# Performance work log

Measured on AMD Instinct MI355X. Metric: run time of the kernel, lower is better.

Reference implementation:

```python
import jax, jax.numpy as jnp
import numpy as np
import math

B, N, D = 64, 128, 128          # graphs, nodes per graph, d_model
D_STATE = 2                     # Mamba default d_state
D_CONV = 4                      # Mamba default conv kernel
DT_RANK = math.ceil(D / 16)     # 8
CUTOFF = 10.0
N_GAUSS = 50                    # GaussianSmearing(0, 10, 50)
EPS_RMS = 1e-5


def setup_inputs() -> dict:
    key = jax.random.key(0)
    ks = jax.random.split(key, 12)
    s = 0.05
    inp = {}
    inp['x'] = jax.random.normal(ks[0], (B * N, D), jnp.float32)
    inp['pos'] = jax.random.normal(ks[1], (B * N, 3), jnp.float32) * 5.0
    inp['map_idx'] = jax.random.randint(ks[2], (B * N,), 0, 16)
    inp['batch'] = jnp.repeat(jnp.arange(B), N)
    # RMSNorm
    inp['norm_w'] = jnp.ones((D,), jnp.float32)
    # simple message-passing gnn (stand-in for injected gnn module)
    inp['gnn_w1'] = jax.random.normal(ks[3], (D, D), jnp.float32) * s
    inp['gnn_b1'] = jnp.zeros((D,), jnp.float32)
    inp['gnn_w2'] = jax.random.normal(ks[4], (D, D), jnp.float32) * s
    inp['gnn_b2'] = jnp.zeros((D,), jnp.float32)
    # Linear(50, 1) on Gaussian-smeared edge distances
    inp['lin_w'] = jax.random.normal(ks[5], (N_GAUSS, 1), jnp.float32) * s
    inp['lin_b'] = jnp.zeros((1,), jnp.float32)
    # MambaBlock params (stored [in, out])
    inp['in_proj_w'] = jax.random.normal(ks[6], (D, 2 * D), jnp.float32) * s
    inp['conv_w'] = jax.random.normal(ks[7], (D, D_CONV), jnp.float32) * s
    inp['conv_b'] = jnp.zeros((D,), jnp.float32)
    inp['x_proj_w'] = jax.random.normal(ks[8], (D, DT_RANK + 2 * D_STATE), jnp.float32) * s
    inp['dt_proj_w'] = jax.random.normal(ks[9], (DT_RANK, D), jnp.float32) * s
    inp['dt_proj_b'] = jnp.zeros((D,), jnp.float32)
    inp['A_log'] = jnp.log(jnp.tile(jnp.arange(1, D_STATE + 1, dtype=jnp.float32), (D, 1)))
    inp['D_param'] = jnp.ones((D,), jnp.float32)
    inp['out_proj_w'] = jax.random.normal(ks[10], (D, D), jnp.float32) * s
    return inp


def _rmsnorm(x, w):
    return x * jax.lax.rsqrt(jnp.mean(x * x, axis=-1, keepdims=True) + EPS_RMS) * w


def _mamba(x_t, adj, in_proj_w, conv_w, conv_b, x_proj_w, dt_proj_w, dt_proj_b,
           A_log, D_param, out_proj_w):
    # x_t: [N, D] node sequence for one graph; adj: [N, N] dense edge-value matrix
    L = x_t.shape[0]
    A = -jnp.exp(A_log)                                   # [D, S]
    xr = x_t @ in_proj_w                                  # [L, 2D]
    xm, res = xr[:, :D], xr[:, D:]
    # causal depthwise conv1d (padding d_conv-1, truncated to L)
    xp = jnp.pad(xm, ((D_CONV - 1, 0), (0, 0)))
    xc = conv_b + sum(xp[j:j + L] * conv_w[:, j] for j in range(D_CONV))
    xc = jax.nn.silu(xc)                                  # [L, D]
    dbl = xc @ x_proj_w                                   # [L, dt_rank + 2S]
    delta = dbl[:, :DT_RANK]
    Bm = dbl[:, DT_RANK:DT_RANK + D_STATE]                # [L, S]
    Cm = dbl[:, DT_RANK + D_STATE:]                       # [L, S]
    delta = jax.nn.softplus(delta @ dt_proj_w + dt_proj_b)  # [L, D]
    # temp_adj_padded: ones [D, D] with adjacency slice in top-left
    m = min(L, D)
    adj_pad = jnp.ones((D, D), dtype=adj.dtype).at[:m, :m].set(adj[:m, :m])
    delta_p = delta @ adj_pad                             # [L, D]
    dA = jnp.exp(delta_p[:, :, None] * A[None])           # [L, D, S]
    dBu = delta_p[:, :, None] * Bm[:, None, :] * xc[:, :, None]

    def step(h, t):
        dA_t, dBu_t, C_t = t
        h = dA_t * h + dBu_t                              # [D, S]
        return h, h @ C_t                                 # [D]

    _, ys = jax.lax.scan(step, jnp.zeros((D, D_STATE), x_t.dtype), (dA, dBu, Cm))
    y = ys + xc * D_param
    y = y * jax.nn.silu(res)
    out = y @ out_proj_w
    return jnp.where(jnp.isfinite(out), out, 0.0)


def reference(x, pos, map_idx, batch, norm_w, gnn_w1, gnn_b1, gnn_w2, gnn_b2,
              lin_w, lin_b, in_proj_w, conv_w, conv_b, x_proj_w, dt_proj_w,
              dt_proj_b, A_log, D_param, out_proj_w):
    x1 = _rmsnorm(x, norm_w)                              # [B*N, D]
    xg = x1.reshape(B, N, D)
    pg = pos.reshape(B, N, 3)
    # per-graph radius graph (dense): dist + edge mask
    diff = pg[:, :, None, :] - pg[:, None, :, :]          # [B, N, N, 3]
    d2 = jnp.sum(diff * diff, axis=-1)
    eye = jnp.eye(N, dtype=bool)[None]
    dist = jnp.sqrt(jnp.where(eye, 1.0, d2))              # safe sqrt on diag
    edge_mask = (~eye) & (dist < CUTOFF)                  # [B, N, N]
    em = edge_mask.astype(x1.dtype)
    # simple message-passing gnn: mean-aggregate relu(Wx) over radius neighbors
    h = jax.nn.relu(xg @ gnn_w1 + gnn_b1)
    deg = jnp.clip(jnp.sum(em, axis=-1, keepdims=True), 1.0, None)
    agg = jnp.einsum('bij,bjd->bid', em, h) / deg
    x2 = agg @ gnn_w2 + gnn_b2                            # [B, N, D]
    # GaussianSmearing(0, 10, 50) + Linear(50, 1) -> dense edge-value matrix
    offsets = jnp.linspace(0.0, 10.0, N_GAUSS)
    coeff = -0.5 / (offsets[1] - offsets[0]) ** 2
    smear = jnp.exp(coeff * (dist[..., None] - offsets) ** 2)  # [B, N, N, 50]
    d_dense = smear @ lin_w[:, 0] + lin_b[0]
    adj = jnp.where(edge_mask, d_dense, 0.0)              # sparse-to-dense
    # Mamba mixer over each graph's node sequence
    mix = jax.vmap(lambda xt, a: _mamba(xt, a, in_proj_w, conv_w, conv_b,
                                        x_proj_w, dt_proj_w, dt_proj_b,
                                        A_log, D_param, out_proj_w))
    x3 = mix(x2, adj).reshape(B * N, D)
    output = x3 + x1
    return (output, pos, map_idx)
```

## Files before the change

### kernel.cpp

```cpp
#include <hip/hip_runtime.h>
#include <math.h>

#define B_ 64
#define N_ 128
#define D_ 128
#define BN_ 8192
#define NG_ 50
#define CUTOFF_ 10.0f

typedef __attribute__((ext_vector_type(8))) short short8v;
typedef __attribute__((ext_vector_type(4))) float f32x4;
#define MFMA16 __builtin_amdgcn_mfma_f32_16x16x32_bf16

__device__ __forceinline__ float bf2f(unsigned short h) {
    return __builtin_bit_cast(float, ((unsigned int)h) << 16);
}
__device__ __forceinline__ unsigned short f2bf(float f) {
    unsigned int u = __builtin_bit_cast(unsigned int, f);
    return (unsigned short)((u + 0x7FFFu + ((u >> 16) & 1u)) >> 16);
}
__device__ __forceinline__ void splitbf(float x, unsigned short& h, unsigned short& l) {
    h = f2bf(x);
    l = f2bf(x - bf2f(h));
}
__device__ __forceinline__ void gl_lds(const void* g, void* l) {
    __builtin_amdgcn_global_load_lds(
        (const __attribute__((address_space(1))) void*)g,
        (__attribute__((address_space(3))) void*)l, 16, 0, 0);
}

__global__ __launch_bounds__(256) void setup_k(
        const float* __restrict__ x, const float* __restrict__ norm_w,
        const float* __restrict__ pos, const int* __restrict__ mi,
        const float* __restrict__ lin_w, const float* __restrict__ lin_b,
        const float* __restrict__ w1, const float* __restrict__ w2,
        const float* __restrict__ b2, const float* __restrict__ in_proj,
        const float* __restrict__ xpw, const float* __restrict__ dtw,
        const float* __restrict__ out_proj,
        unsigned short* __restrict__ w1Th, unsigned short* __restrict__ w1Tl,
        unsigned short* __restrict__ WdTh, unsigned short* __restrict__ WdTl,
        unsigned short* __restrict__ opTh, unsigned short* __restrict__ opTl,
        unsigned short* __restrict__ WfTh, unsigned short* __restrict__ WfTl,
        float* __restrict__ bfv,
        float* __restrict__ x1f, unsigned short* __restrict__ x1h,
        unsigned short* __restrict__ x1l,
        unsigned short* __restrict__ adjh, unsigned short* __restrict__ adjl,
        unsigned short* __restrict__ emh, float* __restrict__ rdeg,
        float* __restrict__ out) {
    int blk = blockIdx.x, t = threadIdx.x;
    if (blk < 513) {
        if (blk < 128) {
            if (t < 128) {
                unsigned short h, l;
                splitbf(w1[blk * 128 + t], h, l);
                w1Th[t * 128 + blk] = h; w1Tl[t * 128 + blk] = l;
            }
        } else if (blk < 256) {
            int m = blk - 128;
            if (t < 128) {
                float s = 0.0f;
                #pragma unroll
                for (int r = 0; r < 8; r++) s = fmaf(xpw[m * 12 + r], dtw[r * 128 + t], s);
                unsigned short h, l; splitbf(s, h, l);
                WdTh[t * 128 + m] = h; WdTl[t * 128 + m] = l;
            }
        } else if (blk < 384) {
            int k = blk - 256;
            if (t < 128) {
                unsigned short h, l;
                splitbf(out_proj[k * 128 + t], h, l);
                opTh[t * 128 + k] = h; opTl[t * 128 + k] = l;
            }
        } else if (blk < 512) {
            int k = blk - 384;
            float s = 0.0f;
            #pragma unroll 8
            for (int j = 0; j < 128; j++) s = fmaf(w2[k * 128 + j], in_proj[j * 256 + t], s);
            unsigned short h, l; splitbf(s, h, l);
            WfTh[t * 128 + k] = h; WfTl[t * 128 + k] = l;
        } else {
            float s = 0.0f;
            #pragma unroll 8
            for (int j = 0; j < 128; j++) s = fmaf(b2[j], in_proj[j * 256 + t], s);
            bfv[t] = s;
        }
    } else if (blk < 642) {
        int idx = (blk - 513) * 256 + t;
        if (idx < BN_ * 3) out[(size_t)BN_ * D_ + idx] = pos[idx];
        if (idx < BN_) out[(size_t)BN_ * D_ + BN_ * 3 + idx] = (float)mi[idx];
    } else if (blk < 2690) {
        int rblk = blk - 642;
        int wv = t >> 6, ln = t & 63;
        int row = rblk * 4 + wv;
        const float2* xr = reinterpret_cast<const float2*>(x) + (size_t)row * 64;
        float2 v = xr[ln];
        float s = fmaf(v.x, v.x, v.y * v.y);
        #pragma unroll
        for (int o = 32; o > 0; o >>= 1) s += __shfl_down(s, o, 64);
        float tot = __shfl(s, 0, 64);
        float r = rsqrtf(tot * (1.0f / D_) + 1e-5f);
        float2 wv2 = reinterpret_cast<const float2*>(norm_w)[ln];
        float o0 = v.x * r * wv2.x, o1 = v.y * r * wv2.y;
        reinterpret_cast<float2*>(x1f)[(size_t)row * 64 + ln] = make_float2(o0, o1);
        unsigned short h0, l0, h1, l1;
        splitbf(o0, h0, l0); splitbf(o1, h1, l1);
        reinterpret_cast<ushort2*>(x1h)[(size_t)row * 64 + ln] = make_ushort2(h0, h1);
        reinterpret_cast<ushort2*>(x1l)[(size_t)row * 64 + ln] = make_ushort2(l0, l1);
    } else {
        __shared__ float px[N_], py[N_], pz[N_];
        __shared__ float lw[NG_];
        __shared__ int degs[8];
        int ablk = blk - 2690;
        int bx = ablk & 15, b = ablk >> 4;
        if (t < N_) {
            const float* p = pos + (size_t)(b * N_ + t) * 3;
            px[t] = p[0]; py[t] = p[1]; pz[t] = p[2];
        } else if (t - N_ < NG_) {
            lw[t - N_] = lin_w[t - N_];
        }
        if (t >= 248) degs[t - 248] = 0;
        __syncthreads();
        float linb = lin_b[0];
        int j = t & 127;
        int il = t >> 7;
        const float DEL = 10.0f / 49.0f;
        const float COEFF = -0.5f / (DEL * DEL);
        #pragma unroll
        for (int p = 0; p < 4; p++) {
            int i = bx * 8 + p * 2 + il;
            float dx = px[i] - px[j], dy = py[i] - py[j], dz = pz[i] - pz[j];
            float d2 = dx * dx + dy * dy + dz * dz;
            float dist = (i == j) ? 1.0f : sqrtf(d2);
            bool edge = (i != j) && (dist < CUTOFF_);
            float val = 0.0f;
            if (edge) {
                int g0 = (int)ceilf((dist - 1.75f) / DEL); if (g0 < 0) g0 = 0;
                int g1 = (int)floorf((dist + 1.75f) / DEL); if (g1 > NG_ - 1) g1 = NG_ - 1;
                float s = linb;
                for (int g = g0; g <= g1; g++) {
                    float tt = dist - (float)g * DEL;
                    s += lw[g] * expf(COEFF * tt * tt);
                }
                val = s;
            }
            size_t idx = ((size_t)b * N_ + i) * N_ + j;
            unsigned short h, l; splitbf(val, h, l);
            adjh[idx] = h; adjl[idx] = l;
            emh[idx] = edge ? 0x3F80 : 0;
            unsigned long long msk = __ballot(edge);
            if ((t & 63) == 0) atomicAdd(&degs[p * 2 + il], __popcll(msk));
        }
        __syncthreads();
        if (t < 8) {
            int dg = degs[t];
            rdeg[(size_t)b * N_ + bx * 8 + t] = 1.0f / (float)(dg > 0 ? dg : 1);
        }
    }
}

#define AHOFF 0
#define ALOFF 8192
#define BHOFF 16384
#define BLOFF 32768
template <int EPI, bool ALO>
__global__ __launch_bounds__(256, 3) void mgemm_k(
        const unsigned short* __restrict__ Ah, const unsigned short* __restrict__ Al,
        const unsigned short* __restrict__ BTh, const unsigned short* __restrict__ BTl,
        const float* __restrict__ bias, const float* __restrict__ AUX,
        float* __restrict__ Cf, unsigned short* __restrict__ Ch,
        unsigned short* __restrict__ Cl, float* __restrict__ Cf2,
        int cstride, int wbs) {
    extern __shared__ char sm[];
    int tid = threadIdx.x;
    int row_base = blockIdx.x * 32;
    int col_base = blockIdx.y * 64;

    const unsigned short* pBh = BTh;
    const unsigned short* pBl = BTl;
    if (wbs) {
        size_t bo = (size_t)(row_base >> 7) * (size_t)wbs;
        pBh += bo; pBl += bo;
    }

    #pragma unroll
    for (int i = 0; i < 2; i++) {
        int s = tid + i * 256;
        int row = s >> 4, inner = s & 15;
        int gb = (inner * 16) ^ ((row & 7) << 4);
        size_t gsrc = (size_t)(row_base + row) * 256 + gb;
        gl_lds((const char*)Ah + gsrc, sm + AHOFF + s * 16);
        if (ALO) gl_lds((const char*)Al + gsrc, sm + ALOFF + s * 16);
    }
    #pragma unroll
    for (int i = 0; i < 4; i++) {
        int s = tid + i * 256;
        int n = s >> 4, inner = s & 15;
        int gb = (inner * 16) ^ ((n & 7) << 4);
        size_t gsrc = (size_t)(col_base + n) * 256 + gb;
        gl_lds((const char*)pBh + gsrc, sm + BHOFF + s * 16);
        gl_lds((const char*)pBl + gsrc, sm + BLOFF + s * 16);
    }
    __syncthreads();

    int w = tid >> 6, l = tid & 63;
    int rlow = l & 15, kb_lane = (l >> 4) * 16;
    int nB = w * 16 + rlow;
    int nswz = (nB & 7) << 4;
    f32x4 acc[2] = {{0.f, 0.f, 0.f, 0.f}, {0.f, 0.f, 0.f, 0.f}};
    #pragma unroll
    for (int kb = 0; kb < 4; kb++) {
        int kbyte = kb * 64 + kb_lane;
        short8v bh = *(const short8v*)(sm + BHOFF + nB * 256 + (kbyte ^ nswz));
        short8v bl = *(const short8v*)(sm + BLOFF + nB * 256 + (kbyte ^ nswz));
        #pragma unroll
        for (int rf = 0; rf < 2; rf++) {
            int ra = rf * 16 + rlow;
            int aswz = (ra & 7) << 4;
            short8v ah = *(const short8v*)(sm + AHOFF + ra * 256 + (kbyte ^ aswz));
            acc[rf] = MFMA16(ah, bh, acc[rf], 0, 0, 0);
            acc[rf] = MFMA16(ah, bl, acc[rf], 0, 0, 0);
            if (ALO) {
                short8v al_ = *(const short8v*)(sm + ALOFF + ra * 256 + (kbyte ^ aswz));
                acc[rf] = MFMA16(al_, bh, acc[rf], 0, 0, 0);
            }
        }
    }

    int colg = col_base + w * 16 + rlow;
    #pragma unroll
    for (int rf = 0; rf < 2; rf++) {
        int row0 = row_base + rf * 16 + (l >> 4) * 4;
        if (EPI == 1) {
            float b_ = bias[colg];
            unsigned short hh[4], ll[4];
            #pragma unroll
            for (int q = 0; q < 4; q++) {
                float t = fmaxf(acc[rf][q] + b_, 0.0f);
                splitbf(t, hh[q], ll[q]);
            }
            size_t bb = (size_t)(row0 >> 7) * 16384 + (size_t)colg * 128 + (row0 & 127);
            *reinterpret_cast<ushort4*>(Ch + bb) = make_ushort4(hh[0], hh[1], hh[2], hh[3]);
            *reinterpret_cast<ushort4*>(Cl + bb) = make_ushort4(ll[0], ll[1], ll[2], ll[3]);
        } else if (EPI == 7) {
            size_t bb = ((size_t)(row0 >> 7) * 128 + colg) * 128 + (row0 & 127);
            *reinterpret_cast<float4*>(Cf + bb) =
                make_float4(acc[rf][0], acc[rf][1], acc[rf][2], acc[rf][3]);
        } else if (EPI == 6 && colg >= 128) {
            float b_ = bias[colg];
            float v[4];
            #pragma unroll
            for (int q = 0; q < 4; q++) {
                float rs = acc[rf][q] + b_;
                v[q] = rs / (1.0f + expf(-rs));
            }
            size_t bb = ((size_t)(row0 >> 7) * 128 + (colg - 128)) * 128 + (row0 & 127);
            *reinterpret_cast<float4*>(Cf2 + bb) = make_float4(v[0], v[1], v[2], v[3]);
        } else {
            #pragma unroll
            for (int q = 0; q < 4; q++) {
                int row = row0 + q;
                float t = acc[rf][q];
                if (EPI == 2) {
                    t *= AUX[row];
                    unsigned short h, lo; splitbf(t, h, lo);
                    Ch[(size_t)row * 128 + colg] = h;
                    Cl[(size_t)row * 128 + colg] = lo;
                }
                if (EPI == 4) {
                    t += bias[colg];
                    t = fmaxf(t, 0.0f) + log1pf(expf(-fabsf(t)));
                    unsigned short h, lo; splitbf(t, h, lo);
                    Ch[(size_t)row * 128 + colg] = h;
                    Cl[(size_t)row * 128 + colg] = lo;
                }
                if (EPI == 5) {
                    t = isfinite(t) ? t : 0.0f;
                    t += AUX[(size_t)row * 128 + colg];
                    Cf[(size_t)row * cstride + colg] = t;
                }
                if (EPI == 6) {
                    t += bias[colg];
                    Cf[(size_t)row * 128 + colg] = t;
                }
            }
        }
    }
}

__global__ __launch_bounds__(256) void convsm_k(const float* __restrict__ xm,
                                                const float* __restrict__ conv_w,
                                                const float* __restrict__ conv_b,
                                                const float* __restrict__ xpw,
                                                unsigned short* __restrict__ xch,
                                                unsigned short* __restrict__ xcl,
                                                float* __restrict__ xcT,
                                                float* __restrict__ bcT) {
    int tid = threadIdx.x;
    int slot = tid >> 7;
    int d = tid & 127;
    int ln = tid & 63;
    int wv = (tid >> 6) & 1;
    __shared__ float red[2][2][4];
    __shared__ float xcs[4][128];
    float cw[4];
    #pragma unroll
    for (int jj = 0; jj < 4; jj++) cw[jj] = conv_w[d * 4 + jj];
    float cb = conv_b[d];
    float4 wv4 = *reinterpret_cast<const float4*>(xpw + d * 12 + 8);

    #pragma unroll
    for (int it = 0; it < 2; it++) {
        int row = blockIdx.x * 4 + it * 2 + slot;
        int bt = row & 127;
        float accv = cb;
        #pragma unroll
        for (int jj = 0; jj < 4; jj++) {
            int tt = bt + jj - 3;
            if (tt >= 0) accv = fmaf(xm[((size_t)(row + jj - 3)) * 128 + d], cw[jj], accv);
        }
        float xcv = accv / (1.0f + expf(-accv));
        xcs[it * 2 + slot][d] = xcv;
        unsigned short h, lo; splitbf(xcv, h, lo);
        xch[(size_t)row * D_ + d] = h;
        xcl[(size_t)row * D_ + d] = lo;
        float p0 = xcv * wv4.x, p1 = xcv * wv4.y, p2 = xcv * wv4.z, p3 = xcv * wv4.w;
        #pragma unroll
        for (int o = 32; o > 0; o >>= 1) {
            p0 += __shfl_down(p0, o, 64);
            p1 += __shfl_down(p1, o, 64);
            p2 += __shfl_down(p2, o, 64);
            p3 += __shfl_down(p3, o, 64);
        }
        if (ln == 0) {
            red[slot][wv][0] = p0; red[slot][wv][1] = p1;
            red[slot][wv][2] = p2; red[slot][wv][3] = p3;
        }
        __syncthreads();
        if (d < 4) {
            int b = row >> 7;
            bcT[(size_t)b * 512 + d * 128 + (row & 127)] = red[slot][0][d] + red[slot][1][d];
        }
        __syncthreads();
    }
    if (tid < 128) {
        int b = blockIdx.x >> 5;
        int t0 = (blockIdx.x * 4) & 127;
        float4 v = make_float4(xcs[0][tid], xcs[1][tid], xcs[2][tid], xcs[3][tid]);
        *reinterpret_cast<float4*>(xcT + ((size_t)b * 128 + tid) * 128 + t0) = v;
    }
}

__global__ __launch_bounds__(256) void scan_k(const float* __restrict__ dpT,
                                              const float* __restrict__ xcT,
                                              const float* __restrict__ bcT,
                                              const float* __restrict__ resT,
                                              const float* __restrict__ A_log,
                                              const float* __restrict__ Dpar,
                                              unsigned short* __restrict__ yh,
                                              unsigned short* __restrict__ yl) {
    int g = blockIdx.x * 256 + threadIdx.x;
    int b = g >> 7, d = g & 127;
    float a1 = -expf(A_log[d * 2]);
    float a2 = -expf(A_log[d * 2 + 1]);
    float Dp = Dpar[d];
    const float4* dp4 = reinterpret_cast<const float4*>(dpT + ((size_t)b * 128 + d) * 128);
    const float4* xc4 = reinterpret_cast<const float4*>(xcT + ((size_t)b * 128 + d) * 128);
    const float4* rr4 = reinterpret_cast<const float4*>(resT + ((size_t)b * 128 + d) * 128);
    const float4* b04 = reinterpret_cast<const float4*>(bcT + (size_t)b * 512);
    const float4* b14 = b04 + 32;
    const float4* c04 = b04 + 64;
    const float4* c14 = b04 + 96;
    float h1 = 0.0f, h2 = 0.0f;
    size_t ybase = (size_t)b * 16384 + d;
    #pragma unroll 4
    for (int tc = 0; tc < 32; tc++) {
        float4 dp = dp4[tc], xc = xc4[tc], rr = rr4[tc];
        float4 bm0 = b04[tc], bm1 = b14[tc], cm0 = c04[tc], cm1 = c14[tc];
        #pragma unroll
        for (int q = 0; q < 4; q++) {
            float dpv = (q == 0) ? dp.x : (q == 1) ? dp.y : (q == 2) ? dp.z : dp.w;
            float xcv = (q == 0) ? xc.x : (q == 1) ? xc.y : (q == 2) ? xc.z : xc.w;
            float rv  = (q == 0) ? rr.x : (q == 1) ? rr.y : (q == 2) ? rr.z : rr.w;
            float bmv0 = (q == 0) ? bm0.x : (q == 1) ? bm0.y : (q == 2) ? bm0.z : bm0.w;
            float bmv1 = (q == 0) ? bm1.x : (q == 1) ? bm1.y : (q == 2) ? bm1.z : bm1.w;
            float cmv0 = (q == 0) ? cm0.x : (q == 1) ? cm0.y : (q == 2) ? cm0.z : cm0.w;
            float cmv1 = (q == 0) ? cm1.x : (q == 1) ? cm1.y : (q == 2) ? cm1.z : cm1.w;
            float e1 = expf(dpv * a1), e2 = expf(dpv * a2);
            float bu = dpv * xcv;
            h1 = fmaf(e1, h1, bu * bmv0);
            h2 = fmaf(e2, h2, bu * bmv1);
            float y = fmaf(h1, cmv0, h2 * cmv1);
            float yv = fmaf(xcv, Dp, y) * rv;
            unsigned short hh, ll; splitbf(yv, hh, ll);
            int t = tc * 4 + q;
            yh[ybase + (size_t)t * 128] = hh;
            yl[ybase + (size_t)t * 128] = ll;
        }
    }
}

extern "C" void kernel_launch(void* const* d_in, const int* in_sizes, int n_in,
                              void* d_out, int out_size, void* d_ws, size_t ws_size,
                              hipStream_t stream) {
    const float* x        = (const float*)d_in[0];
    const float* pos      = (const float*)d_in[1];
    const int*   mi       = (const int*)d_in[2];
    const float* norm_w   = (const float*)d_in[4];
    const float* w1       = (const float*)d_in[5];
    const float* b1       = (const float*)d_in[6];
    const float* w2       = (const float*)d_in[7];
    const float* b2       = (const float*)d_in[8];
    const float* lin_w    = (const float*)d_in[9];
    const float* lin_b    = (const float*)d_in[10];
    const float* in_proj  = (const float*)d_in[11];
    const float* conv_w   = (const float*)d_in[12];
    const float* conv_b   = (const float*)d_in[13];
    const float* xpw      = (const float*)d_in[14];
    const float* dtw      = (const float*)d_in[15];
    const float* dtb      = (const float*)d_in[16];
    const float* A_log    = (const float*)d_in[17];
    const float* Dpar     = (const float*)d_in[18];
    const float* out_proj = (const float*)d_in[19];

    float* out = (float*)d_out;
    char* base = (char*)d_ws;
    const size_t MB = 1u << 20;
    const size_t PL = 1048576;

    float* x1f  = (float*)(base);
    float* xm   = (float*)(base + 4 * MB);
    float* resT = (float*)(base + 8 * MB);
    float* dpT  = (float*)(base + 12 * MB);
    float* xcT  = (float*)(base + 16 * MB);
    float* bcT  = (float*)(base + 20 * MB);
    float* rdeg = (float*)(base + 20 * MB + 131072);

    unsigned short* P = (unsigned short*)(base + 21 * MB);
    unsigned short* x1h  = P +  0 * PL;
    unsigned short* x1l  = P +  1 * PL;
    unsigned short* hTh  = P +  2 * PL;
    unsigned short* hTl  = P +  3 * PL;
    unsigned short* aggh = P +  4 * PL;
    unsigned short* aggl = P +  5 * PL;
    unsigned short* xch  = P +  6 * PL;
    unsigned short* xcl  = P +  7 * PL;
    unsigned short* dlh  = P +  8 * PL;
    unsigned short* dll  = P +  9 * PL;
    unsigned short* yh   = P + 10 * PL;
    unsigned short* yl   = P + 11 * PL;
    unsigned short* adjh = P + 12 * PL;
    unsigned short* adjl = P + 13 * PL;
    unsigned short* emh  = P + 14 * PL;

    unsigned short* W = (unsigned short*)(base + 52 * MB);
    unsigned short* w1Th = W;
    unsigned short* w1Tl = W + 16384;
    unsigned short* WdTh = W + 2 * 16384;
    unsigned short* WdTl = W + 3 * 16384;
    unsigned short* opTh = W + 4 * 16384;
    unsigned short* opTl = W + 5 * 16384;
    unsigned short* WfTh = W + 6 * 16384;
    unsigned short* WfTl = WfTh + 32768;
    float* bfv = (float*)(WfTl + 32768);

    const size_t gsm = 49152;

    setup_k<<<3714, 256, 0, stream>>>(x, norm_w, pos, mi, lin_w, lin_b,
                                      w1, w2, b2, in_proj, xpw, dtw, out_proj,
                                      w1Th, w1Tl, WdTh, WdTl, opTh, opTl, WfTh, WfTl,
                                      bfv, x1f, x1h, x1l, adjh, adjl, emh, rdeg, out);
    mgemm_k<1, true><<<dim3(256, 2), 256, gsm, stream>>>(
        x1h, x1l, w1Th, w1Tl, b1, nullptr, nullptr, hTh, hTl, nullptr, 128, 0);
    mgemm_k<2, false><<<dim3(256, 2), 256, gsm, stream>>>(
        emh, emh, hTh, hTl, nullptr, rdeg, nullptr, aggh, aggl, nullptr, 128, 16384);
    mgemm_k<6, true><<<dim3(256, 4), 256, gsm, stream>>>(
        aggh, aggl, WfTh, WfTl, bfv, nullptr, xm, nullptr, nullptr, resT, 128, 0);
    convsm_k<<<2048, 256, 0, stream>>>(xm, conv_w, conv_b, xpw, xch, xcl, xcT, bcT);
    mgemm_k<4, true><<<dim3(256, 2), 256, gsm, stream>>>(
        xch, xcl, WdTh, WdTl, dtb, nullptr, nullptr, dlh, dll, nullptr, 128, 0);
    mgemm_k<7, true><<<dim3(256, 2), 256, gsm, stream>>>(
        dlh, dll, adjh, adjl, nullptr, nullptr, dpT, nullptr, nullptr, nullptr, 128, 16384);
    scan_k<<<32, 256, 0, stream>>>(dpT, xcT, bcT, resT, A_log, Dpar, yh, yl);
    mgemm_k<5, true><<<dim3(256, 2), 256, gsm, stream>>>(
        yh, yl, opTh, opTl, nullptr, x1f, out, nullptr, nullptr, nullptr, 128, 0);
}
```

Baseline: 95.70 us.

## Fuse in_proj, conv+SiLU, dt projection and adjacency GEMM into one kernel

Replaces four launches (the in_proj GEMM, the conv/SiLU/x_proj kernel, the dt_proj softplus GEMM and the adjacency GEMM) with one 512-thread kernel. Each block owns a 32-row tile of one graph and keeps the intermediates (xm, the xc split-bf16 planes, delta) in 160KB of LDS. A 16-row halo is recomputed so the causal conv can run locally. This removes several global round trips and launch gaps. In exchange it redundantly computes halo rows, uses 256 large-LDS blocks with limited occupancy, and serializes the stages inside each block.

```diff
diff --git a/kernel.cpp b/kernel.cpp
--- a/kernel.cpp
+++ b/kernel.cpp
@@ -168,8 +168,7 @@
         const unsigned short* __restrict__ BTh, const unsigned short* __restrict__ BTl,
         const float* __restrict__ bias, const float* __restrict__ AUX,
         float* __restrict__ Cf, unsigned short* __restrict__ Ch,
-        unsigned short* __restrict__ Cl, float* __restrict__ Cf2,
-        int cstride, int wbs) {
+        unsigned short* __restrict__ Cl, int cstride, int wbs) {
     extern __shared__ char sm[];
     int tid = threadIdx.x;
     int row_base = blockIdx.x * 32;
@@ -241,20 +240,6 @@
             size_t bb = (size_t)(row0 >> 7) * 16384 + (size_t)colg * 128 + (row0 & 127);
             *reinterpret_cast<ushort4*>(Ch + bb) = make_ushort4(hh[0], hh[1], hh[2], hh[3]);
             *reinterpret_cast<ushort4*>(Cl + bb) = make_ushort4(ll[0], ll[1], ll[2], ll[3]);
-        } else if (EPI == 7) {
-            size_t bb = ((size_t)(row0 >> 7) * 128 + colg) * 128 + (row0 & 127);
-            *reinterpret_cast<float4*>(Cf + bb) =
-                make_float4(acc[rf][0], acc[rf][1], acc[rf][2], acc[rf][3]);
-        } else if (EPI == 6 && colg >= 128) {
-            float b_ = bias[colg];
-            float v[4];
-            #pragma unroll
-            for (int q = 0; q < 4; q++) {
-                float rs = acc[rf][q] + b_;
-                v[q] = rs / (1.0f + expf(-rs));
-            }
-            size_t bb = ((size_t)(row0 >> 7) * 128 + (colg - 128)) * 128 + (row0 & 127);
-            *reinterpret_cast<float4*>(Cf2 + bb) = make_float4(v[0], v[1], v[2], v[3]);
         } else {
             #pragma unroll
             for (int q = 0; q < 4; q++) {
@@ -266,87 +251,215 @@
                     Ch[(size_t)row * 128 + colg] = h;
                     Cl[(size_t)row * 128 + colg] = lo;
                 }
-                if (EPI == 4) {
-                    t += bias[colg];
-                    t = fmaxf(t, 0.0f) + log1pf(expf(-fabsf(t)));
-                    unsigned short h, lo; splitbf(t, h, lo);
-                    Ch[(size_t)row * 128 + colg] = h;
-                    Cl[(size_t)row * 128 + colg] = lo;
-                }
                 if (EPI == 5) {
                     t = isfinite(t) ? t : 0.0f;
                     t += AUX[(size_t)row * 128 + colg];
                     Cf[(size_t)row * cstride + colg] = t;
                 }
-                if (EPI == 6) {
-                    t += bias[colg];
-                    Cf[(size_t)row * 128 + colg] = t;
+            }
+        }
+    }
+}
+
+__device__ __forceinline__ void st128(char* dst, const char* g, int tid) {
+    #pragma unroll
+    for (int i = 0; i < 4; i++) {
+        int s = tid + i * 512;
+        int row = s >> 4, inner = s & 15;
+        gl_lds(g + row * 256 + ((inner * 16) ^ ((row & 7) << 4)), dst + s * 16);
+    }
+}
+__device__ __forceinline__ void stA48(char* dst, const char* g, int r0, int tid) {
+    #pragma unroll
+    for (int i = 0; i < 2; i++) {
+        int s = tid + i * 512;
+        if (s < 768) {
+            int lr = s >> 4, inner = s & 15;
+            int srow = r0 - 16 + lr; if (srow < 0) srow = 0;
+            gl_lds(g + srow * 256 + ((inner * 16) ^ ((lr & 7) << 4)), dst + s * 16);
+        }
+    }
+}
+template <int NRF>
+__device__ __forceinline__ void fpass(const char* sm, int ah, int al, int bh, int bl,
+                                      int w, int l, f32x4 (&acc)[NRF]) {
+    int rlow = l & 15, khi = (l >> 4) * 16;
+    int nB = w * 16 + rlow;
+    int nkey = (nB & 7) << 4;
+    #pragma unroll
+    for (int kb = 0; kb < 4; kb++) {
+        int kbyte = kb * 64 + khi;
+        short8v bhv = *(const short8v*)(sm + bh + nB * 256 + (kbyte ^ nkey));
+        short8v blv = *(const short8v*)(sm + bl + nB * 256 + (kbyte ^ nkey));
+        #pragma unroll
+        for (int rf = 0; rf < NRF; rf++) {
+            int ra = rf * 16 + rlow;
+            int ao = ra * 256 + (kbyte ^ ((ra & 7) << 4));
+            short8v ahv = *(const short8v*)(sm + ah + ao);
+            short8v alv = *(const short8v*)(sm + al + ao);
+            acc[rf] = MFMA16(ahv, bhv, acc[rf], 0, 0, 0);
+            acc[rf] = MFMA16(ahv, blv, acc[rf], 0, 0, 0);
+            acc[rf] = MFMA16(alv, bhv, acc[rf], 0, 0, 0);
+        }
+    }
+}
+
+__global__ __launch_bounds__(512, 2) void fused_k(
+        const unsigned short* __restrict__ aggh, const unsigned short* __restrict__ aggl,
+        const unsigned short* __restrict__ WfTh, const unsigned short* __restrict__ WfTl,
+        const float* __restrict__ bfv,
+        const float* __restrict__ conv_w, const float* __restrict__ conv_b,
+        const float* __restrict__ xpw,
+        const unsigned short* __restrict__ WdTh, const unsigned short* __restrict__ WdTl,
+        const float* __restrict__ dtb,
+        const unsigned short* __restrict__ adjh, const unsigned short* __restrict__ adjl,
+        float* __restrict__ resT, float* __restrict__ xcT,
+        float* __restrict__ bcT, float* __restrict__ dpT) {
+    __shared__ __align__(16) char sm[163840];
+    const int AH = 0, AL = 12288, XM = 24576, BH = 49152, BL = 81920,
+              XCH = 114688, XCL = 122880, DH = 131072, DL = 139264, XCF = 147456;
+    int blk = blockIdx.x, tid = threadIdx.x;
+    int b = blk >> 2, r0 = (blk & 3) * 32;
+    int w = tid >> 6, l = tid & 63;
+    int rlow = l & 15, qrow = (l >> 4) * 4;
+
+    stA48(sm + AH, (const char*)aggh + (size_t)b * 32768, r0, tid);
+    stA48(sm + AL, (const char*)aggl + (size_t)b * 32768, r0, tid);
+    st128(sm + BH, (const char*)WfTh, tid);
+    st128(sm + BL, (const char*)WfTl, tid);
+    __syncthreads();
+
+    f32x4 acc[3] = {{0.f,0.f,0.f,0.f},{0.f,0.f,0.f,0.f},{0.f,0.f,0.f,0.f}};
+    fpass<3>(sm, AH, AL, BH, BL, w, l, acc);
+    __syncthreads();
+    st128(sm + BH, (const char*)WfTh + 32768, tid);
+    st128(sm + BL, (const char*)WfTl + 32768, tid);
+    {
+        int colg = w * 16 + rlow;
+        float bb = bfv[colg];
+        #pragma unroll
+        for (int rf = 0; rf < 3; rf++) {
+            #pragma unroll
+            for (int q = 0; q < 4; q++) {
+                int lr = rf * 16 + qrow + q;
+                *(float*)(sm + XM + lr * 512 + ((colg * 4) ^ ((lr & 7) << 4))) =
+                    acc[rf][q] + bb;
+            }
+        }
+    }
+    __syncthreads();
+
+    f32x4 acc2[3] = {{0.f,0.f,0.f,0.f},{0.f,0.f,0.f,0.f},{0.f,0.f,0.f,0.f}};
+    fpass<3>(sm, AH, AL, BH, BL, w, l, acc2);
+    {
+        int colg = w * 16 + rlow;
+        float bb = bfv[128 + colg];
+        #pragma unroll
+        for (int rf = 1; rf < 3; rf++) {
+            int lr0 = rf * 16 + qrow;
+            int tt = r0 + lr0 - 16;
+            float v[4];
+            #pragma unroll
+            for (int q = 0; q < 4; q++) {
+                float rs = acc2[rf][q] + bb;
+                v[q] = rs / (1.0f + expf(-rs));
+            }
+            *reinterpret_cast<float4*>(resT + ((size_t)b * 128 + colg) * 128 + tt) =
+                make_float4(v[0], v[1], v[2], v[3]);
+        }
+    }
+    __syncthreads();
+
+    st128(sm + BH, (const char*)WdTh, tid);
+    st128(sm + BL, (const char*)WdTl, tid);
+    {
+        int ot = tid >> 4, dg = tid & 15;
+        float pc0 = 0, pc1 = 0, pc2 = 0, pc3 = 0;
+        #pragma unroll
+        for (int k = 0; k < 8; k++) {
+            int d = dg * 8 + k;
+            float accv = conv_b[d];
+            #pragma unroll
+            for (int jj = 0; jj < 4; jj++) {
+                int tt = r0 + ot + jj - 3;
+                if (tt >= 0) {
+                    int lr = ot + jj - 3 + 16;
+                    float xv = *(const float*)(sm + XM + lr * 512 +
+                                               ((d * 4) ^ ((lr & 7) << 4)));
+                    accv = fmaf(xv, conv_w[d * 4 + jj], accv);
                 }
             }
-        }
-    }
-}
-
-__global__ __launch_bounds__(256) void convsm_k(const float* __restrict__ xm,
-                                                const float* __restrict__ conv_w,
-                                                const float* __restrict__ conv_b,
-                                                const float* __restrict__ xpw,
-                                                unsigned short* __restrict__ xch,
-                                                unsigned short* __restrict__ xcl,
-                                                float* __restrict__ xcT,
-                                                float* __restrict__ bcT) {
-    int tid = threadIdx.x;
-    int slot = tid >> 7;
-    int d = tid & 127;
-    int ln = tid & 63;
-    int wv = (tid >> 6) & 1;
-    __shared__ float red[2][2][4];
-    __shared__ float xcs[4][128];
-    float cw[4];
-    #pragma unroll
-    for (int jj = 0; jj < 4; jj++) cw[jj] = conv_w[d * 4 + jj];
-    float cb = conv_b[d];
-    float4 wv4 = *reinterpret_cast<const float4*>(xpw + d * 12 + 8);
-
-    #pragma unroll
-    for (int it = 0; it < 2; it++) {
-        int row = blockIdx.x * 4 + it * 2 + slot;
-        int bt = row & 127;
-        float accv = cb;
-        #pragma unroll
-        for (int jj = 0; jj < 4; jj++) {
-            int tt = bt + jj - 3;
-            if (tt >= 0) accv = fmaf(xm[((size_t)(row + jj - 3)) * 128 + d], cw[jj], accv);
-        }
-        float xcv = accv / (1.0f + expf(-accv));
-        xcs[it * 2 + slot][d] = xcv;
-        unsigned short h, lo; splitbf(xcv, h, lo);
-        xch[(size_t)row * D_ + d] = h;
-        xcl[(size_t)row * D_ + d] = lo;
-        float p0 = xcv * wv4.x, p1 = xcv * wv4.y, p2 = xcv * wv4.z, p3 = xcv * wv4.w;
-        #pragma unroll
-        for (int o = 32; o > 0; o >>= 1) {
-            p0 += __shfl_down(p0, o, 64);
-            p1 += __shfl_down(p1, o, 64);
-            p2 += __shfl_down(p2, o, 64);
-            p3 += __shfl_down(p3, o, 64);
-        }
-        if (ln == 0) {
-            red[slot][wv][0] = p0; red[slot][wv][1] = p1;
-            red[slot][wv][2] = p2; red[slot][wv][3] = p3;
-        }
-        __syncthreads();
-        if (d < 4) {
-            int b = row >> 7;
-            bcT[(size_t)b * 512 + d * 128 + (row & 127)] = red[slot][0][d] + red[slot][1][d];
-        }
-        __syncthreads();
-    }
-    if (tid < 128) {
-        int b = blockIdx.x >> 5;
-        int t0 = (blockIdx.x * 4) & 127;
-        float4 v = make_float4(xcs[0][tid], xcs[1][tid], xcs[2][tid], xcs[3][tid]);
-        *reinterpret_cast<float4*>(xcT + ((size_t)b * 128 + tid) * 128 + t0) = v;
+            float xc = accv / (1.0f + expf(-accv));
+            unsigned short hh, ll; splitbf(xc, hh, ll);
+            int pb = ot * 256 + ((d * 2) ^ ((ot & 7) << 4));
+            *(unsigned short*)(sm + XCH + pb) = hh;
+            *(unsigned short*)(sm + XCL + pb) = ll;
+            *(float*)(sm + XCF + ot * 512 + ((d * 4) ^ ((ot & 7) << 4))) = xc;
+            float4 xw = *(const float4*)(xpw + d * 12 + 8);
+            pc0 = fmaf(xc, xw.x, pc0); pc1 = fmaf(xc, xw.y, pc1);
+            pc2 = fmaf(xc, xw.z, pc2); pc3 = fmaf(xc, xw.w, pc3);
+        }
+        #pragma unroll
+        for (int m = 1; m < 16; m <<= 1) {
+            pc0 += __shfl_xor(pc0, m, 64);
+            pc1 += __shfl_xor(pc1, m, 64);
+            pc2 += __shfl_xor(pc2, m, 64);
+            pc3 += __shfl_xor(pc3, m, 64);
+        }
+        if (dg < 4) {
+            float pv = dg == 0 ? pc0 : dg == 1 ? pc1 : dg == 2 ? pc2 : pc3;
+            bcT[(size_t)b * 512 + dg * 128 + r0 + ot] = pv;
+        }
+    }
+    __syncthreads();
+
+    {
+        int d = tid & 127, tg = tid >> 7;
+        float v[8];
+        #pragma unroll
+        for (int k = 0; k < 8; k++) {
+            int ot = tg * 8 + k;
+            v[k] = *(const float*)(sm + XCF + ot * 512 + ((d * 4) ^ ((ot & 7) << 4)));
+        }
+        float* dst = xcT + ((size_t)b * 128 + d) * 128 + r0 + tg * 8;
+        *reinterpret_cast<float4*>(dst) = make_float4(v[0], v[1], v[2], v[3]);
+        *reinterpret_cast<float4*>(dst + 4) = make_float4(v[4], v[5], v[6], v[7]);
+    }
+
+    f32x4 dacc[2] = {{0.f,0.f,0.f,0.f},{0.f,0.f,0.f,0.f}};
+    fpass<2>(sm, XCH, XCL, BH, BL, w, l, dacc);
+    {
+        int colg = w * 16 + rlow;
+        float db = dtb[colg];
+        #pragma unroll
+        for (int rf = 0; rf < 2; rf++) {
+            #pragma unroll
+            for (int q = 0; q < 4; q++) {
+                int lr = rf * 16 + qrow + q;
+                float t = dacc[rf][q] + db;
+                t = fmaxf(t, 0.0f) + log1pf(expf(-fabsf(t)));
+                unsigned short hh, ll; splitbf(t, hh, ll);
+                int pb = lr * 256 + ((colg * 2) ^ ((lr & 7) << 4));
+                *(unsigned short*)(sm + DH + pb) = hh;
+                *(unsigned short*)(sm + DL + pb) = ll;
+            }
+        }
+    }
+    __syncthreads();
+
+    st128(sm + BH, (const char*)adjh + (size_t)b * 32768, tid);
+    st128(sm + BL, (const char*)adjl + (size_t)b * 32768, tid);
+    __syncthreads();
+    f32x4 pacc[2] = {{0.f,0.f,0.f,0.f},{0.f,0.f,0.f,0.f}};
+    fpass<2>(sm, DH, DL, BH, BL, w, l, pacc);
+    {
+        int colg = w * 16 + rlow;
+        #pragma unroll
+        for (int rf = 0; rf < 2; rf++) {
+            int lr0 = rf * 16 + qrow;
+            *reinterpret_cast<float4*>(dpT + ((size_t)b * 128 + colg) * 128 + r0 + lr0) =
+                make_float4(pacc[rf][0], pacc[rf][1], pacc[rf][2], pacc[rf][3]);
+        }
     }
 }
 
@@ -428,7 +541,6 @@
     const size_t PL = 1048576;
 
     float* x1f  = (float*)(base);
-    float* xm   = (float*)(base + 4 * MB);
     float* resT = (float*)(base + 8 * MB);
     float* dpT  = (float*)(base + 12 * MB);
     float* xcT  = (float*)(base + 16 * MB);
@@ -442,10 +554,6 @@
     unsigned short* hTl  = P +  3 * PL;
     unsigned short* aggh = P +  4 * PL;
     unsigned short* aggl = P +  5 * PL;
-    unsigned short* xch  = P +  6 * PL;
-    unsigned short* xcl  = P +  7 * PL;
-    unsigned short* dlh  = P +  8 * PL;
-    unsigned short* dll  = P +  9 * PL;
     unsigned short* yh   = P + 10 * PL;
     unsigned short* yl   = P + 11 * PL;
     unsigned short* adjh = P + 12 * PL;
@@ -470,17 +578,13 @@
                                       w1Th, w1Tl, WdTh, WdTl, opTh, opTl, WfTh, WfTl,
                                       bfv, x1f, x1h, x1l, adjh, adjl, emh, rdeg, out);
     mgemm_k<1, true><<<dim3(256, 2), 256, gsm, stream>>>(
-        x1h, x1l, w1Th, w1Tl, b1, nullptr, nullptr, hTh, hTl, nullptr, 128, 0);
+        x1h, x1l, w1Th, w1Tl, b1, nullptr, nullptr, hTh, hTl, 128, 0);
     mgemm_k<2, false><<<dim3(256, 2), 256, gsm, stream>>>(
-        emh, emh, hTh, hTl, nullptr, rdeg, nullptr, aggh, aggl, nullptr, 128, 16384);
-    mgemm_k<6, true><<<dim3(256, 4), 256, gsm, stream>>>(
-        aggh, aggl, WfTh, WfTl, bfv, nullptr, xm, nullptr, nullptr, resT, 128, 0);
-    convsm_k<<<2048, 256, 0, stream>>>(xm, conv_w, conv_b, xpw, xch, xcl, xcT, bcT);
-    mgemm_k<4, true><<<dim3(256, 2), 256, gsm, stream>>>(
-        xch, xcl, WdTh, WdTl, dtb, nullptr, nullptr, dlh, dll, nullptr, 128, 0);
-    mgemm_k<7, true><<<dim3(256, 2), 256, gsm, stream>>>(
-        dlh, dll, adjh, adjl, nullptr, nullptr, dpT, nullptr, nullptr, nullptr, 128, 16384);
+        emh, emh, hTh, hTl, nullptr, rdeg, nullptr, aggh, aggl, 128, 16384);
+    fused_k<<<256, 512, 0, stream>>>(aggh, aggl, WfTh, WfTl, bfv,
+                                     conv_w, conv_b, xpw, WdTh, WdTl, dtb,
+                                     adjh, adjl, resT, xcT, bcT, dpT);
     scan_k<<<32, 256, 0, stream>>>(dpT, xcT, bcT, resT, A_log, Dpar, yh, yl);
     mgemm_k<5, true><<<dim3(256, 2), 256, gsm, stream>>>(
-        yh, yl, opTh, opTl, nullptr, x1f, out, nullptr, nullptr, nullptr, 128, 0);
-}
+        yh, yl, opTh, opTl, nullptr, x1f, out, nullptr, nullptr, 128, 0);
+}
```

New measurement: 93.47 us. 2.3% less time.
